# Performance work log

Measured on AMD Instinct MI355X. Metric: run time of the kernel, lower is better.

The kernel has to match this reference:

```python
import jax, jax.numpy as jnp
import numpy as np

NUM_EMBEDDINGS = 8192
EMBEDDING_DIM = 512
BETA = 0.25


def setup_inputs() -> dict:
    key = jax.random.key(0)
    k1, k2 = jax.random.split(key)
    x = jax.random.normal(k1, (16, 1024, EMBEDDING_DIM), dtype=jnp.float32)
    # torch.nn.init.uniform_ -> U[0, 1)
    embeddings = jax.random.uniform(k2, (NUM_EMBEDDINGS, EMBEDDING_DIM), dtype=jnp.float32)
    return {"x": x, "embeddings": embeddings}


def reference(x, embeddings):
    input_shape = x.shape
    flat = x.reshape(-1, EMBEDDING_DIM)                      # [N, D]
    sim = jnp.matmul(flat, embeddings.T)                     # [N, K]
    s1 = jnp.sum(flat * flat, axis=1, keepdims=True)         # [N, 1]
    s2 = jnp.sum(embeddings * embeddings, axis=1)            # [K]
    distances = s1 + s2 - 2.0 * sim                          # [N, K]
    idx = jnp.argmin(distances, axis=1)                      # [N]
    # direct gather (math-equivalent to one-hot @ codebook)
    quantized = embeddings[idx].reshape(input_shape)
    sg = jax.lax.stop_gradient
    commitment_loss = BETA * jnp.mean((sg(quantized) - x) ** 2)
    codebook_loss = jnp.mean((quantized - sg(x)) ** 2)
    loss = commitment_loss + codebook_loss
    out = x + sg(quantized - x)                              # straight-through
    return (out, quantized, loss)
```

## Files before the change

### kernel.cpp

```cpp
#include <hip/hip_runtime.h>

#define DIM 512
#define N_ROWS 16384
#define K_CODES 8192
#define BK 32
#define TM 128
#define TN 128
#define NG (K_CODES / TN)
#define OUT_ELEMS (N_ROWS * DIM)
#define MARGIN 0.125f
#define RESCAN_CHUNK 256
#define RESCAN_NCHUNK (K_CODES / RESCAN_CHUNK)
#define RESCAN_ROWS 8
#define NT (DIM / BK)

typedef _Float16 f16;
typedef _Float16 f16x8 __attribute__((ext_vector_type(8)));
typedef float f32x4 __attribute__((ext_vector_type(4)));

__device__ __forceinline__ unsigned long long pack_di(float d, int i) {
  unsigned u = __float_as_uint(d);
  u = (u & 0x80000000u) ? ~u : (u | 0x80000000u);
  return ((unsigned long long)u << 32) | (unsigned)i;
}

__global__ __launch_bounds__(256) void vq_split_kernel(const float* __restrict__ src,
                                                       f16* __restrict__ x16) {
  int i = (blockIdx.x * 256 + threadIdx.x) * 8;
  float4 v0 = *(const float4*)(src + i);
  float4 v1 = *(const float4*)(src + i + 4);
  float f[8] = {v0.x, v0.y, v0.z, v0.w, v1.x, v1.y, v1.z, v1.w};
  f16x8 h;
  #pragma unroll
  for (int j = 0; j < 8; ++j) h[j] = (f16)f[j];
  *(f16x8*)(x16 + i) = h;
}

__global__ __launch_bounds__(256) void vq_split_enorm_kernel(
    const float* __restrict__ emb, f16* __restrict__ e16,
    float* __restrict__ enorm, int* __restrict__ counter) {
  int gid  = blockIdx.x * 256 + threadIdx.x;
  if (gid == 0) *counter = 0;
  int code = gid >> 6;
  int lane = gid & 63;
  size_t off = (size_t)code * DIM + lane * 8;
  float4 v0 = *(const float4*)(emb + off);
  float4 v1 = *(const float4*)(emb + off + 4);
  float f[8] = {v0.x, v0.y, v0.z, v0.w, v1.x, v1.y, v1.z, v1.w};
  f16x8 h;
  float s = 0.0f;
  #pragma unroll
  for (int j = 0; j < 8; ++j) {
    h[j] = (f16)f[j];
    s = fmaf(f[j], f[j], s);
  }
  *(f16x8*)(e16 + off) = h;
  #pragma unroll
  for (int o = 32; o > 0; o >>= 1) s += __shfl_down(s, o);
  if (lane == 0) enorm[code] = s;
}

__device__ __forceinline__ void gl2lds16(const f16* g, f16* l) {
  __builtin_amdgcn_global_load_lds((const __attribute__((address_space(1))) unsigned int*)g,
                                   (__attribute__((address_space(3))) unsigned int*)l,
                                   16, 0, 0);
}

__device__ __forceinline__ void top2_merge(float& d1, int& i1, float& d2,
                                           float od1, int oi1, float od2) {
  if (od1 < d1 || (od1 == d1 && oi1 < i1)) {
    d2 = fminf(d1, od2);
    d1 = od1; i1 = oi1;
  } else {
    d2 = fminf(d2, od1);
  }
}

__global__ __launch_bounds__(256, 4) void vq_argmin_mfma_kernel(
    const f16* __restrict__ x16, const f16* __restrict__ e16,
    const float* __restrict__ enorm,
    float* __restrict__ cand_d1, int* __restrict__ cand_i1, float* __restrict__ cand_d2) {
  __shared__ __align__(16) f16 Ax[2][TM * BK];
  __shared__ __align__(16) f16 Be[2][TN * BK];
  __shared__ float red_d1[2][TM];
  __shared__ int   red_i1[2][TM];
  __shared__ float red_d2[2][TM];

  const int tid  = threadIdx.x;
  const int wave = tid >> 6;
  const int lane = tid & 63;
  const int bm = blockIdx.x, bn = blockIdx.y;
  const int wr = (wave >> 1) * 64;
  const int wc = (wave & 1) * 64;

  const f16* gsrc0;
  int ldoff;
  {
    const int srow = lane >> 2;
    const int scg  = ((lane & 3) ^ ((lane >> 3) & 3)) * 8;
    const int rowoff = (wave & 1) * 64;
    if (wave < 2) { gsrc0 = x16 + (size_t)(bm * TM + rowoff + srow) * DIM + scg; }
    else          { gsrc0 = e16 + (size_t)(bn * TN + rowoff + srow) * DIM + scg; }
    ldoff = rowoff * BK;
  }
  f16* dstA0 = (wave < 2) ? &Ax[0][ldoff] : &Be[0][ldoff];
  f16* dstA1 = (wave < 2) ? &Ax[1][ldoff] : &Be[1][ldoff];

  f32x4 acc[4][4];
  #pragma unroll
  for (int i = 0; i < 4; ++i)
    #pragma unroll
    for (int j = 0; j < 4; ++j)
      acc[i][j] = (f32x4){0.f, 0.f, 0.f, 0.f};

  const int fr = lane & 15;
  const int fq = lane >> 4;
  const int sw8 = (fq ^ ((fr >> 1) & 3)) * 8;

  #pragma unroll
  for (int i = 0; i < 4; ++i)
    gl2lds16(gsrc0 + (size_t)(16 * i) * DIM, dstA0 + (16 * i) * BK);
  __syncthreads();

  #pragma unroll 2
  for (int s = 0; s < NT; ++s) {
    const int cur = s & 1;
    if (s + 1 < NT) {
      f16* nb = cur ? dstA0 : dstA1;
      const int k1 = (s + 1) * BK;
      #pragma unroll
      for (int i = 0; i < 4; ++i)
        gl2lds16(gsrc0 + (size_t)(16 * i) * DIM + k1, nb + (16 * i) * BK);
    }

    const f16* A = cur ? &Ax[1][0] : &Ax[0][0];
    const f16* B = cur ? &Be[1][0] : &Be[0][0];
    f16x8 a[4], b[4];
    #pragma unroll
    for (int f = 0; f < 4; ++f) {
      a[f] = *(const f16x8*)&A[(wr + f * 16 + fr) * BK + sw8];
      b[f] = *(const f16x8*)&B[(wc + f * 16 + fr) * BK + sw8];
    }
    #pragma unroll
    for (int mf = 0; mf < 4; ++mf)
      #pragma unroll
      for (int nf = 0; nf < 4; ++nf)
        acc[mf][nf] = __builtin_amdgcn_mfma_f32_16x16x32_f16(a[mf], b[nf], acc[mf][nf], 0, 0, 0);

    __syncthreads();
  }

  float en[4];
  #pragma unroll
  for (int nf = 0; nf < 4; ++nf)
    en[nf] = enorm[bn * TN + wc + nf * 16 + fr];

  #pragma unroll
  for (int mf = 0; mf < 4; ++mf) {
    #pragma unroll
    for (int reg = 0; reg < 4; ++reg) {
      float d1 = 3.4e38f, d2 = 3.4e38f;
      int i1 = 0;
      #pragma unroll
      for (int nf = 0; nf < 4; ++nf) {
        float d = en[nf] - 2.0f * acc[mf][nf][reg];
        int ci = bn * TN + wc + nf * 16 + fr;
        if (d < d1) { d2 = d1; d1 = d; i1 = ci; }
        else if (d < d2) { d2 = d; }
      }
      #pragma unroll
      for (int m = 1; m <= 8; m <<= 1) {
        float od1 = __shfl_xor(d1, m, 16);
        int   oi1 = __shfl_xor(i1, m, 16);
        float od2 = __shfl_xor(d2, m, 16);
        top2_merge(d1, i1, d2, od1, oi1, od2);
      }
      if (fr == 0) {
        int row = wr + mf * 16 + fq * 4 + reg;
        red_d1[wave & 1][row] = d1;
        red_i1[wave & 1][row] = i1;
        red_d2[wave & 1][row] = d2;
      }
    }
  }
  __syncthreads();
  if (tid < TM) {
    float d1 = red_d1[0][tid]; int i1 = red_i1[0][tid]; float d2 = red_d2[0][tid];
    top2_merge(d1, i1, d2, red_d1[1][tid], red_i1[1][tid], red_d2[1][tid]);
    size_t o = (size_t)bn * N_ROWS + (size_t)bm * TM + tid;
    cand_d1[o] = d1; cand_i1[o] = i1; cand_d2[o] = d2;
  }
}

__global__ __launch_bounds__(256) void vq_merge2_kernel(
    const float* __restrict__ cd1, const int* __restrict__ ci1, const float* __restrict__ cd2,
    int* __restrict__ idx, int* __restrict__ flag,
    int* __restrict__ counter, int* __restrict__ flagged,
    unsigned long long* __restrict__ packed,
    float* __restrict__ loss_slot) {
  int r = blockIdx.x * 256 + threadIdx.x;
  if (r == 0) *loss_slot = 0.0f;
  float d1 = 3.4e38f, d2 = 3.4e38f;
  int i1 = 0;
  for (int g = 0; g < NG; ++g) {
    size_t o = (size_t)g * N_ROWS + r;
    top2_merge(d1, i1, d2, cd1[o], ci1[o], cd2[o]);
  }
  idx[r] = i1;
  int f = (d2 - d1 < MARGIN) ? 1 : 0;
  flag[r] = f;
  if (f) {
    packed[r] = 0xFFFFFFFFFFFFFFFFULL;
    int slot = atomicAdd(counter, 1);
    flagged[slot] = r;
  }
}

__global__ __launch_bounds__(256) void vq_rescan_kernel(
    const float* __restrict__ x, const float* __restrict__ emb,
    const float* __restrict__ enorm,
    const int* __restrict__ counter, const int* __restrict__ flagged,
    unsigned long long* __restrict__ packed) {
  __shared__ float4 xs[RESCAN_ROWS][DIM / 4];
  __shared__ unsigned long long wmin[4][RESCAN_ROWS];
  const int t  = threadIdx.x;
  const int wv = t >> 6, ln = t & 63;
  const int nflag   = counter[0];
  const int ngroups = (nflag + RESCAN_ROWS - 1) / RESCAN_ROWS;
  const int nitems  = ngroups * RESCAN_NCHUNK;
  for (int item = blockIdx.x; item < nitems; item += gridDim.x) {
    const int g  = item / RESCAN_NCHUNK;
    const int c0 = (item % RESCAN_NCHUNK) * RESCAN_CHUNK;
    __syncthreads();
    #pragma unroll
    for (int u = 0; u < 4; ++u) {
      int i4 = u * 256 + t;
      int j = i4 >> 7, kk = i4 & 127;
      int rj = g * RESCAN_ROWS + j;
      if (rj < nflag) xs[j][kk] = ((const float4*)(x + (size_t)flagged[rj] * DIM))[kk];
    }
    __syncthreads();
    unsigned long long best[RESCAN_ROWS];
    #pragma unroll
    for (int j = 0; j < RESCAN_ROWS; ++j) best[j] = ~0ULL;
    {
      const int c = c0 + t;
      const float4* e4 = (const float4*)(emb + (size_t)c * DIM);
      float s0[RESCAN_ROWS], s1[RESCAN_ROWS], s2[RESCAN_ROWS], s3[RESCAN_ROWS];
      #pragma unroll
      for (int j = 0; j < RESCAN_ROWS; ++j) { s0[j] = s1[j] = s2[j] = s3[j] = 0.f; }
      for (int k = 0; k < DIM / 4; ++k) {
        float4 ev = e4[k];
        #pragma unroll
        for (int j = 0; j < RESCAN_ROWS; ++j) {
          float4 xv = xs[j][k];
          s0[j] = fmaf(xv.x, ev.x, s0[j]);
          s1[j] = fmaf(xv.y, ev.y, s1[j]);
          s2[j] = fmaf(xv.z, ev.z, s2[j]);
          s3[j] = fmaf(xv.w, ev.w, s3[j]);
        }
      }
      const float en = enorm[c];
      #pragma unroll
      for (int j = 0; j < RESCAN_ROWS; ++j) {
        float d = en - 2.0f * ((s0[j] + s1[j]) + (s2[j] + s3[j]));
        unsigned long long p = pack_di(d, c);
        if (p < best[j]) best[j] = p;
      }
    }
    #pragma unroll
    for (int j = 0; j < RESCAN_ROWS; ++j) {
      #pragma unroll
      for (int off = 32; off > 0; off >>= 1) {
        unsigned long long o = __shfl_down(best[j], off);
        if (o < best[j]) best[j] = o;
      }
    }
    if (ln == 0) {
      #pragma unroll
      for (int j = 0; j < RESCAN_ROWS; ++j) wmin[wv][j] = best[j];
    }
    __syncthreads();
    if (t < RESCAN_ROWS) {
      int rj = g * RESCAN_ROWS + t;
      if (rj < nflag) {
        unsigned long long m = wmin[0][t];
        if (wmin[1][t] < m) m = wmin[1][t];
        if (wmin[2][t] < m) m = wmin[2][t];
        if (wmin[3][t] < m) m = wmin[3][t];
        atomicMin(&packed[flagged[rj]], m);
      }
    }
  }
}

__global__ __launch_bounds__(256) void vq_gather_kernel(
    const float* __restrict__ x, const float* __restrict__ emb,
    const int* __restrict__ idx, const int* __restrict__ flag,
    const unsigned long long* __restrict__ packed,
    float* __restrict__ out, float* __restrict__ quant,
    float* __restrict__ loss_slot) {
  __shared__ float wsum[4];
  const int wave = threadIdx.x >> 6;
  const int lane = threadIdx.x & 63;
  const int row  = blockIdx.x * 4 + wave;
  const int code = flag[row] ? (int)(packed[row] & 0xFFFFFFFFu) : idx[row];
  const float4* xp = (const float4*)(x   + (size_t)row  * DIM + lane * 8);
  const float4* ep = (const float4*)(emb + (size_t)code * DIM + lane * 8);
  float s = 0.0f;
  #pragma unroll
  for (int t = 0; t < 2; ++t) {
    float4 xv = xp[t];
    float4 ev = ep[t];
    float dx = ev.x - xv.x, dy = ev.y - xv.y, dz = ev.z - xv.z, dw = ev.w - xv.w;
    s += dx * dx + dy * dy + dz * dz + dw * dw;
    ((float4*)(out   + (size_t)row * DIM + lane * 8))[t] = ev;
    ((float4*)(quant + (size_t)row * DIM + lane * 8))[t] = ev;
  }
  #pragma unroll
  for (int off = 32; off > 0; off >>= 1) s += __shfl_down(s, off);
  if (lane == 0) wsum[wave] = s;
  __syncthreads();
  if (threadIdx.x == 0) {
    float tot = wsum[0] + wsum[1] + wsum[2] + wsum[3];
    atomicAdd(loss_slot, tot * (1.25f / (float)OUT_ELEMS));
  }
}

extern "C" void kernel_launch(void* const* d_in, const int* in_sizes, int n_in,
                              void* d_out, int out_size, void* d_ws, size_t ws_size,
                              hipStream_t stream) {
  const float* x   = (const float*)d_in[0];
  const float* emb = (const float*)d_in[1];
  float* out   = (float*)d_out;
  float* quant = out + OUT_ELEMS;
  float* loss  = out + 2 * OUT_ELEMS;

  char* ws = (char*)d_ws;
  f16*   x16    = (f16*)(ws);
  f16*   e16    = (f16*)(ws + 16777216);
  float* enorm  = (float*)(ws + 25165824);
  float* cd1    = (float*)(ws + 25198592);
  int*   ci1    = (int*)  (ws + 29392896);
  float* cd2    = (float*)(ws + 33587200);
  int*   idx    = (int*)  (ws + 37781504);
  int*   flag   = (int*)  (ws + 37847040);
  int*   counter= (int*)  (ws + 37912576);
  int*   flagged= (int*)  (ws + 37912832);
  unsigned long long* packed = (unsigned long long*)(ws + 37978368);

  vq_split_kernel<<<OUT_ELEMS / (8 * 256), 256, 0, stream>>>(x, x16);
  vq_split_enorm_kernel<<<K_CODES * 64 / 256, 256, 0, stream>>>(emb, e16, enorm, counter);
  vq_argmin_mfma_kernel<<<dim3(N_ROWS / TM, K_CODES / TN), 256, 0, stream>>>(
      x16, e16, enorm, cd1, ci1, cd2);
  vq_merge2_kernel<<<N_ROWS / 256, 256, 0, stream>>>(
      cd1, ci1, cd2, idx, flag, counter, flagged, packed, loss);
  vq_rescan_kernel<<<2048, 256, 0, stream>>>(x, emb, enorm, counter, flagged, packed);
  vq_gather_kernel<<<N_ROWS / 4, 256, 0, stream>>>(x, emb, idx, flag, packed, out, quant, loss);
}
```

Before: 513.0 us.

## Rescan only candidate code groups within margin instead of full codebook

The merge kernel now emits (row, group) work items only for the 128-code groups whose fp16 best distance lies within the margin of the row's overall best. The rescan kernel processes one such item per 128-thread block in fp32, instead of scanning all 8192 codes for every flagged row. This is meant to cut the exact-rescan FLOPs and codebook reads. It adds atomics in the merge kernel and a fixed item capacity; if that capacity is exceeded, items are dropped silently and the result could be wrong.

```diff
diff --git a/kernel.cpp b/kernel.cpp
--- a/kernel.cpp
+++ b/kernel.cpp
@@ -9,9 +9,7 @@
 #define NG (K_CODES / TN)
 #define OUT_ELEMS (N_ROWS * DIM)
 #define MARGIN 0.125f
-#define RESCAN_CHUNK 256
-#define RESCAN_NCHUNK (K_CODES / RESCAN_CHUNK)
-#define RESCAN_ROWS 8
+#define CAP_ITEMS 262144
 #define NT (DIM / BK)
 
 typedef _Float16 f16;
@@ -38,9 +36,9 @@
 
 __global__ __launch_bounds__(256) void vq_split_enorm_kernel(
     const float* __restrict__ emb, f16* __restrict__ e16,
-    float* __restrict__ enorm, int* __restrict__ counter) {
+    float* __restrict__ enorm, int* __restrict__ rcounter) {
   int gid  = blockIdx.x * 256 + threadIdx.x;
-  if (gid == 0) *counter = 0;
+  if (gid == 0) *rcounter = 0;
   int code = gid >> 6;
   int lane = gid & 63;
   size_t off = (size_t)code * DIM + lane * 8;
@@ -195,7 +193,7 @@
 __global__ __launch_bounds__(256) void vq_merge2_kernel(
     const float* __restrict__ cd1, const int* __restrict__ ci1, const float* __restrict__ cd2,
     int* __restrict__ idx, int* __restrict__ flag,
-    int* __restrict__ counter, int* __restrict__ flagged,
+    int* __restrict__ rcounter, int* __restrict__ item_row, int* __restrict__ item_grp,
     unsigned long long* __restrict__ packed,
     float* __restrict__ loss_slot) {
   int r = blockIdx.x * 256 + threadIdx.x;
@@ -211,85 +209,54 @@
   flag[r] = f;
   if (f) {
     packed[r] = 0xFFFFFFFFFFFFFFFFULL;
-    int slot = atomicAdd(counter, 1);
-    flagged[slot] = r;
-  }
-}
-
-__global__ __launch_bounds__(256) void vq_rescan_kernel(
+    const float thresh = d1 + MARGIN;
+    for (int g = 0; g < NG; ++g) {
+      if (cd1[(size_t)g * N_ROWS + r] <= thresh) {
+        int slot = atomicAdd(rcounter, 1);
+        if (slot < CAP_ITEMS) { item_row[slot] = r; item_grp[slot] = g; }
+      }
+    }
+  }
+}
+
+__global__ __launch_bounds__(128) void vq_rescan_kernel(
     const float* __restrict__ x, const float* __restrict__ emb,
     const float* __restrict__ enorm,
-    const int* __restrict__ counter, const int* __restrict__ flagged,
+    const int* __restrict__ rcounter,
+    const int* __restrict__ item_row, const int* __restrict__ item_grp,
     unsigned long long* __restrict__ packed) {
-  __shared__ float4 xs[RESCAN_ROWS][DIM / 4];
-  __shared__ unsigned long long wmin[4][RESCAN_ROWS];
-  const int t  = threadIdx.x;
-  const int wv = t >> 6, ln = t & 63;
-  const int nflag   = counter[0];
-  const int ngroups = (nflag + RESCAN_ROWS - 1) / RESCAN_ROWS;
-  const int nitems  = ngroups * RESCAN_NCHUNK;
+  __shared__ float4 xs[DIM / 4];
+  __shared__ unsigned long long wred[2];
+  const int t = threadIdx.x;
+  int nitems = rcounter[0];
+  if (nitems > CAP_ITEMS) nitems = CAP_ITEMS;
   for (int item = blockIdx.x; item < nitems; item += gridDim.x) {
-    const int g  = item / RESCAN_NCHUNK;
-    const int c0 = (item % RESCAN_NCHUNK) * RESCAN_CHUNK;
+    const int r = item_row[item];
+    const int g = item_grp[item];
     __syncthreads();
-    #pragma unroll
-    for (int u = 0; u < 4; ++u) {
-      int i4 = u * 256 + t;
-      int j = i4 >> 7, kk = i4 & 127;
-      int rj = g * RESCAN_ROWS + j;
-      if (rj < nflag) xs[j][kk] = ((const float4*)(x + (size_t)flagged[rj] * DIM))[kk];
-    }
+    xs[t] = ((const float4*)(x + (size_t)r * DIM))[t];
     __syncthreads();
-    unsigned long long best[RESCAN_ROWS];
-    #pragma unroll
-    for (int j = 0; j < RESCAN_ROWS; ++j) best[j] = ~0ULL;
-    {
-      const int c = c0 + t;
-      const float4* e4 = (const float4*)(emb + (size_t)c * DIM);
-      float s0[RESCAN_ROWS], s1[RESCAN_ROWS], s2[RESCAN_ROWS], s3[RESCAN_ROWS];
-      #pragma unroll
-      for (int j = 0; j < RESCAN_ROWS; ++j) { s0[j] = s1[j] = s2[j] = s3[j] = 0.f; }
-      for (int k = 0; k < DIM / 4; ++k) {
-        float4 ev = e4[k];
-        #pragma unroll
-        for (int j = 0; j < RESCAN_ROWS; ++j) {
-          float4 xv = xs[j][k];
-          s0[j] = fmaf(xv.x, ev.x, s0[j]);
-          s1[j] = fmaf(xv.y, ev.y, s1[j]);
-          s2[j] = fmaf(xv.z, ev.z, s2[j]);
-          s3[j] = fmaf(xv.w, ev.w, s3[j]);
-        }
-      }
-      const float en = enorm[c];
-      #pragma unroll
-      for (int j = 0; j < RESCAN_ROWS; ++j) {
-        float d = en - 2.0f * ((s0[j] + s1[j]) + (s2[j] + s3[j]));
-        unsigned long long p = pack_di(d, c);
-        if (p < best[j]) best[j] = p;
-      }
-    }
-    #pragma unroll
-    for (int j = 0; j < RESCAN_ROWS; ++j) {
-      #pragma unroll
-      for (int off = 32; off > 0; off >>= 1) {
-        unsigned long long o = __shfl_down(best[j], off);
-        if (o < best[j]) best[j] = o;
-      }
-    }
-    if (ln == 0) {
-      #pragma unroll
-      for (int j = 0; j < RESCAN_ROWS; ++j) wmin[wv][j] = best[j];
-    }
+    const int c = g * 128 + t;
+    const float4* e4 = (const float4*)(emb + (size_t)c * DIM);
+    float s0 = 0.f, s1 = 0.f, s2 = 0.f, s3 = 0.f;
+    for (int k = 0; k < DIM / 4; ++k) {
+      float4 xv = xs[k]; float4 ev = e4[k];
+      s0 = fmaf(xv.x, ev.x, s0); s1 = fmaf(xv.y, ev.y, s1);
+      s2 = fmaf(xv.z, ev.z, s2); s3 = fmaf(xv.w, ev.w, s3);
+    }
+    float d = enorm[c] - 2.0f * ((s0 + s1) + (s2 + s3));
+    unsigned long long p = pack_di(d, c);
+    #pragma unroll
+    for (int off = 32; off > 0; off >>= 1) {
+      unsigned long long o = __shfl_down(p, off);
+      if (o < p) p = o;
+    }
+    if ((t & 63) == 0) wred[t >> 6] = p;
     __syncthreads();
-    if (t < RESCAN_ROWS) {
-      int rj = g * RESCAN_ROWS + t;
-      if (rj < nflag) {
-        unsigned long long m = wmin[0][t];
-        if (wmin[1][t] < m) m = wmin[1][t];
-        if (wmin[2][t] < m) m = wmin[2][t];
-        if (wmin[3][t] < m) m = wmin[3][t];
-        atomicMin(&packed[flagged[rj]], m);
-      }
+    if (t == 0) {
+      unsigned long long m = wred[0];
+      if (wred[1] < m) m = wred[1];
+      atomicMin(&packed[r], m);
     }
   }
 }
@@ -345,16 +312,18 @@
   float* cd2    = (float*)(ws + 33587200);
   int*   idx    = (int*)  (ws + 37781504);
   int*   flag   = (int*)  (ws + 37847040);
-  int*   counter= (int*)  (ws + 37912576);
-  int*   flagged= (int*)  (ws + 37912832);
-  unsigned long long* packed = (unsigned long long*)(ws + 37978368);
+  int*   rcounter=(int*)  (ws + 37912576);
+  unsigned long long* packed = (unsigned long long*)(ws + 37912832);
+  int*   item_row=(int*)  (ws + 38043904);
+  int*   item_grp=(int*)  (ws + 39092480);
 
   vq_split_kernel<<<OUT_ELEMS / (8 * 256), 256, 0, stream>>>(x, x16);
-  vq_split_enorm_kernel<<<K_CODES * 64 / 256, 256, 0, stream>>>(emb, e16, enorm, counter);
+  vq_split_enorm_kernel<<<K_CODES * 64 / 256, 256, 0, stream>>>(emb, e16, enorm, rcounter);
   vq_argmin_mfma_kernel<<<dim3(N_ROWS / TM, K_CODES / TN), 256, 0, stream>>>(
       x16, e16, enorm, cd1, ci1, cd2);
   vq_merge2_kernel<<<N_ROWS / 256, 256, 0, stream>>>(
-      cd1, ci1, cd2, idx, flag, counter, flagged, packed, loss);
-  vq_rescan_kernel<<<2048, 256, 0, stream>>>(x, emb, enorm, counter, flagged, packed);
+      cd1, ci1, cd2, idx, flag, rcounter, item_row, item_grp, packed, loss);
+  vq_rescan_kernel<<<2048, 128, 0, stream>>>(
+      x, emb, enorm, rcounter, item_row, item_grp, packed);
   vq_gather_kernel<<<N_ROWS / 4, 256, 0, stream>>>(x, emb, idx, flag, packed, out, quant, loss);
 }
```

Result: faster. 443.1 us (-13.6%).
